# Kernel optimization log

Measured on AMD Instinct MI355X. Metric: run time of the kernel, lower is better.

Reference implementation:

```python
import jax, jax.numpy as jnp
import numpy as np

N, E, F, HID, OUT, B, HEADS = 4096, 131072, 64, 64, 86, 16, 4


def setup_inputs() -> dict:
    key = jax.random.key(0)
    ks = jax.random.split(key, 12)
    s = 0.1
    return {
        "x": jax.random.normal(ks[0], (N, F), dtype=jnp.float32),
        "edge_index": jax.random.randint(ks[1], (2, E), 0, N),
        "edge_attr": jax.random.uniform(ks[2], (E,), dtype=jnp.float32),
        "batch": jnp.sort(jax.random.randint(ks[3], (N,), 0, B)).astype(jnp.int32),
        # GCNConv1: Linear(F -> HID, no bias) + post-aggregation bias
        "W1": jax.random.normal(ks[4], (HID, F), dtype=jnp.float32) * s,
        "b1": jnp.zeros((HID,), jnp.float32),
        # MultiheadAttention(embed_dim=HID, num_heads=4)
        "Win": jax.random.normal(ks[5], (3 * HID, HID), dtype=jnp.float32) * s,
        "b_in": jnp.zeros((3 * HID,), jnp.float32),
        "Wout": jax.random.normal(ks[6], (HID, HID), dtype=jnp.float32) * s,
        "b_out": jnp.zeros((HID,), jnp.float32),
        # GCNConv2: Linear(HID -> OUT)
        "W2": jax.random.normal(ks[7], (OUT, HID), dtype=jnp.float32) * s,
        "b2": jnp.zeros((OUT,), jnp.float32),
    }


def _gcn_layer(h, W, b, src_a, dst_a, norm, n):
    # x' = scatter_add(norm * (x W^T)[src] -> dst) + b   (PyG GCNConv)
    h = h @ W.T
    agg = jax.ops.segment_sum(norm[:, None] * h[src_a], dst_a, num_segments=n)
    return agg + b


def reference(x, edge_index, edge_attr, batch, W1, b1, Win, b_in, Wout, b_out, W2, b2):
    n = x.shape[0]
    # torch.cat([x[:, :-1], x[:, -1:].view(-1,1)], dim=1) == x (identity)
    src, dst = edge_index[0], edge_index[1]
    loop = jnp.arange(n)
    src_a = jnp.concatenate([src, loop])
    dst_a = jnp.concatenate([dst, loop])
    w_a = jnp.concatenate([edge_attr, jnp.ones((n,), x.dtype)])  # self-loops weight 1
    deg = jax.ops.segment_sum(w_a, dst_a, num_segments=n)
    dis = jnp.where(deg > 0, jax.lax.rsqrt(jnp.maximum(deg, 1e-12)), 0.0)
    norm = dis[src_a] * w_a * dis[dst_a]

    h = jax.nn.relu(_gcn_layer(x, W1, b1, src_a, dst_a, norm, n))  # [N, HID]

    # MultiheadAttention over the whole node set as one sequence (batch=1)
    qkv = h @ Win.T + b_in
    q, k, v = jnp.split(qkv, 3, axis=-1)
    dh = HID // HEADS
    to_heads = lambda t: t.reshape(n, HEADS, dh).transpose(1, 0, 2)  # [H, N, dh]
    q, k, v = to_heads(q), to_heads(k), to_heads(v)
    scores = jnp.einsum("hnd,hmd->hnm", q, k) * (1.0 / np.sqrt(dh))
    att = jax.nn.softmax(scores, axis=-1)
    o = jnp.einsum("hnm,hmd->hnd", att, v).transpose(1, 0, 2).reshape(n, HID)
    o = o @ Wout.T + b_out

    h2 = _gcn_layer(o, W2, b2, src_a, dst_a, norm, n)  # [N, OUT]

    # global_mean_pool over graph ids
    sums = jax.ops.segment_sum(h2, batch, num_segments=B)
    cnt = jax.ops.segment_sum(jnp.ones((n,), h2.dtype), batch, num_segments=B)
    return sums / jnp.maximum(cnt, 1.0)[:, None]
```

## Files before the change

### kernel.cpp

```cpp
#include <hip/hip_runtime.h>
#include <hip/hip_bf16.h>

constexpr int N = 4096, E = 131072, OUTF = 86, NB = 16, HEADS = 4, DH = 16;
constexpr int CAP = 128;
constexpr int NSPLIT = 4, KEYS = N / NSPLIT;
constexpr int PCKS = 8;

typedef __attribute__((ext_vector_type(8))) short short8;
typedef __attribute__((ext_vector_type(4))) float f32x4;

constexpr unsigned long long PK_MASK = (1ULL << 40) - 1;
constexpr float PK_SCALE = 1.0f / 16777216.0f;

constexpr size_t OFF_PCK   = 0;
constexpr size_t OFF_INV   = OFF_PCK + 16 * (size_t)N;
constexpr size_t OFF_BUFA  = OFF_INV + 16;
constexpr size_t OFF_QP    = OFF_BUFA + (size_t)N * 64;
constexpr size_t OFF_KP    = OFF_QP + (size_t)N * 32;
constexpr size_t OFF_VP    = OFF_KP + (size_t)N * 32;
constexpr size_t OFF_H2    = OFF_VP + (size_t)N * 32;
constexpr size_t OFF_EPAIR = OFF_H2 + (size_t)N * 86;
constexpr size_t OFF_NORMV = OFF_EPAIR + (size_t)2 * N * CAP;
constexpr size_t OFF_OPART = OFF_NORMV + (size_t)N * CAP;
constexpr size_t OFF_LPART = OFF_OPART + (size_t)HEADS * N * NSPLIT * 16;

__device__ inline unsigned short f2bf(float f) {
    unsigned u = __builtin_bit_cast(unsigned, f);
    u += 0x7FFFu + ((u >> 16) & 1u);
    return (unsigned short)(u >> 16);
}

__device__ inline unsigned pk2bf(float a, float b) {
    __hip_bfloat162 h2 = __float22bfloat162_rn(make_float2(a, b));
    union { __hip_bfloat162 h; unsigned u; } c;
    c.h = h2;
    return c.u;
}

__device__ inline float pk_deg(unsigned long long pk) {
    return (float)(pk & PK_MASK) * PK_SCALE;
}

__global__ __launch_bounds__(256) void d1_kernel(const float* __restrict__ x,
        const float* __restrict__ W1, const int* __restrict__ ei,
        const float* __restrict__ ea, const int* __restrict__ batch,
        const float* __restrict__ b2, float* __restrict__ ws, float* __restrict__ out) {
    __shared__ float4 Ws4[64 * 17];
    __shared__ float4 As4[16 * 17];
    __shared__ int bnd[NB + 1];
    int blk = blockIdx.x, tid = threadIdx.x;
    if (blk < 256) {
        float* bufA = ws + OFF_BUFA;
        for (int idx = tid; idx < 64 * 16; idx += 256)
            Ws4[(idx >> 4) * 17 + (idx & 15)] = ((const float4*)W1)[idx];
        {
            int r = tid >> 4, k4 = tid & 15;
            As4[r * 17 + k4] = ((const float4*)x)[(size_t)(blk * 16 + r) * 16 + k4];
        }
        __syncthreads();
        int r2 = tid & 7, cg = tid >> 3;
        float acc[2][2] = {};
#pragma unroll
        for (int k4 = 0; k4 < 16; ++k4) {
            float4 a0 = As4[r2 * 17 + k4], a1 = As4[(r2 + 8) * 17 + k4];
#pragma unroll
            for (int i = 0; i < 2; ++i) {
                float4 w = Ws4[(cg + 32 * i) * 17 + k4];
                acc[0][i] += a0.x * w.x + a0.y * w.y + a0.z * w.z + a0.w * w.w;
                acc[1][i] += a1.x * w.x + a1.y * w.y + a1.z * w.z + a1.w * w.w;
            }
        }
#pragma unroll
        for (int j = 0; j < 2; ++j)
#pragma unroll
            for (int i = 0; i < 2; ++i)
                bufA[(size_t)(blk * 16 + r2 + 8 * j) * 64 + cg + 32 * i] = acc[j][i];
    } else if (blk < 512) {
        unsigned long long* pck = (unsigned long long*)(ws + OFF_PCK);
        int2* epair = (int2*)(ws + OFF_EPAIR);
        int f = (blk - 256) * 256 + tid;
        int e0 = f, e1 = f + E / 2;
        int s0 = ei[e0], d0 = ei[E + e0];
        int s1 = ei[e1], d1 = ei[E + e1];
        float w0 = ea[e0], w1 = ea[e1];
        unsigned long long a0 = (1ULL << 40) + (unsigned long long)(unsigned)(w0 * 16777216.0f + 0.5f);
        unsigned long long a1 = (1ULL << 40) + (unsigned long long)(unsigned)(w1 * 16777216.0f + 0.5f);
        unsigned long long o0 = atomicAdd(&pck[(size_t)d0 * PCKS], a0);
        unsigned long long o1 = atomicAdd(&pck[(size_t)d1 * PCKS], a1);
        int p0 = (int)(o0 >> 40), p1 = (int)(o1 >> 40);
        if (p0 < CAP) epair[(size_t)d0 * CAP + p0] = make_int2(s0, __float_as_int(w0));
        if (p1 < CAP) epair[(size_t)d1 * CAP + p1] = make_int2(s1, __float_as_int(w1));
    } else {
        float* invcnt = ws + OFF_INV;
        if (tid <= NB) {
            int b = tid, lo = 0, hi = N;
            while (lo < hi) { int m = (lo + hi) >> 1; if (batch[m] < b) lo = m + 1; else hi = m; }
            bnd[tid] = lo;
        }
        __syncthreads();
        if (tid < NB) {
            int cnt = bnd[tid + 1] - bnd[tid];
            invcnt[tid] = cnt > 0 ? 1.0f / (float)cnt : 0.0f;
        }
        for (int idx = tid; idx < NB * OUTF; idx += 256) {
            int b = idx / OUTF;
            int cnt = bnd[b + 1] - bnd[b];
            out[idx] = cnt > 0 ? b2[idx - b * OUTF] : 0.0f;
        }
    }
}

__global__ __launch_bounds__(1024) void d23_kernel(const float* __restrict__ Win,
        const float* __restrict__ b1, const float* __restrict__ b_in,
        float* __restrict__ ws) {
    __shared__ float4 Ws4[16 * 200];
    __shared__ float  Af[16 * 68];

    const unsigned long long* pck = (const unsigned long long*)(ws + OFF_PCK);
    const int2*  epair = (const int2*)(ws + OFF_EPAIR);
    float*       normv = ws + OFF_NORMV;
    const float* bufA  = ws + OFF_BUFA;
    unsigned short* Qp = (unsigned short*)(ws + OFF_QP);
    unsigned short* Kp = (unsigned short*)(ws + OFF_KP);
    unsigned short* Vp = (unsigned short*)(ws + OFF_VP);

    const int tid = threadIdx.x, lane = tid & 63, wv = tid >> 6;
    for (int idx = tid; idx < 192 * 16; idx += 1024) {
        int c = idx >> 4, k4 = idx & 15;
        Ws4[k4 * 200 + c] = ((const float4*)Win)[idx];
    }

    const int node = blockIdx.x * 16 + wv;
    {
        const unsigned long long pkn = pck[(size_t)node * PCKS];
        const float di = rsqrtf(pk_deg(pkn) + 1.0f);
        float acc0 = (di * di) * bufA[(size_t)node * 64 + lane];
        float acc1 = 0.f, acc2 = 0.f, acc3 = 0.f;
        const int cnt = min((int)(pkn >> 40), CAP);
        const int2* pe = epair + (size_t)node * CAP;
        for (int base = 0; base < cnt; base += 64) {
            int rem = cnt - base;
            int   sl = 0;
            float nl = 0.f;
            if (lane < rem) {
                int2 e = pe[base + lane];
                sl = e.x;
                float w = __int_as_float(e.y);
                nl = rsqrtf(pk_deg(pck[(size_t)sl * PCKS]) + 1.0f) * w * di;
                normv[(size_t)node * CAP + base + lane] = nl;
            }
            int m = rem < 64 ? rem : 64;
            int j = 0;
            for (; j + 8 <= m; j += 8) {
                int   s0 = __shfl(sl, j),     s1 = __shfl(sl, j + 1);
                int   s2 = __shfl(sl, j + 2), s3 = __shfl(sl, j + 3);
                int   s4 = __shfl(sl, j + 4), s5 = __shfl(sl, j + 5);
                int   s6 = __shfl(sl, j + 6), s7 = __shfl(sl, j + 7);
                float n0 = __shfl(nl, j),     n1 = __shfl(nl, j + 1);
                float n2 = __shfl(nl, j + 2), n3 = __shfl(nl, j + 3);
                float n4 = __shfl(nl, j + 4), n5 = __shfl(nl, j + 5);
                float n6 = __shfl(nl, j + 6), n7 = __shfl(nl, j + 7);
                float v0 = bufA[(size_t)s0 * 64 + lane], v1 = bufA[(size_t)s1 * 64 + lane];
                float v2 = bufA[(size_t)s2 * 64 + lane], v3 = bufA[(size_t)s3 * 64 + lane];
                float v4 = bufA[(size_t)s4 * 64 + lane], v5 = bufA[(size_t)s5 * 64 + lane];
                float v6 = bufA[(size_t)s6 * 64 + lane], v7 = bufA[(size_t)s7 * 64 + lane];
                acc0 += n0 * v0; acc1 += n1 * v1; acc2 += n2 * v2; acc3 += n3 * v3;
                acc0 += n4 * v4; acc1 += n5 * v5; acc2 += n6 * v6; acc3 += n7 * v7;
            }
            for (; j + 4 <= m; j += 4) {
                int   s0 = __shfl(sl, j),     s1 = __shfl(sl, j + 1);
                int   s2 = __shfl(sl, j + 2), s3 = __shfl(sl, j + 3);
                float n0 = __shfl(nl, j),     n1 = __shfl(nl, j + 1);
                float n2 = __shfl(nl, j + 2), n3 = __shfl(nl, j + 3);
                acc0 += n0 * bufA[(size_t)s0 * 64 + lane];
                acc1 += n1 * bufA[(size_t)s1 * 64 + lane];
                acc2 += n2 * bufA[(size_t)s2 * 64 + lane];
                acc3 += n3 * bufA[(size_t)s3 * 64 + lane];
            }
            for (; j < m; ++j) {
                int   s0 = __shfl(sl, j);
                float n0 = __shfl(nl, j);
                acc0 += n0 * bufA[(size_t)s0 * 64 + lane];
            }
        }
        Af[wv * 68 + lane] = fmaxf((acc0 + acc1) + (acc2 + acc3) + b1[lane], 0.0f);
    }
    __syncthreads();

    {
        const float4* Af4 = (const float4*)Af;
        float acc[3];
#pragma unroll
        for (int i = 0; i < 3; ++i) acc[i] = b_in[lane + 64 * i];
#pragma unroll
        for (int k4 = 0; k4 < 16; ++k4) {
            float4 a = Af4[wv * 17 + k4];
#pragma unroll
            for (int i = 0; i < 3; ++i) {
                float4 w = Ws4[k4 * 200 + lane + 64 * i];
                acc[i] += a.x * w.x + a.y * w.y + a.z * w.z + a.w * w.w;
            }
        }
        const int row = node;
#pragma unroll
        for (int i = 0; i < 3; ++i) {
            int c = lane + 64 * i;
            float v = acc[i];
            if (c < 64) {
                int h = c >> 4, d = c & 15;
                Qp[((size_t)h * N + row) * 16 + d] = f2bf(v * 0.25f);
            } else if (c < 128) {
                int c2 = c - 64, h = c2 >> 4, d = c2 & 15;
                Kp[((size_t)h * N + row) * 16 + d] = f2bf(v);
            } else {
                int c2 = c - 128, h = c2 >> 4, d = c2 & 15;
                Vp[((size_t)h * 16 + d) * N + row] = f2bf(v);
            }
        }
    }
}

__global__ __launch_bounds__(1024) void attn_kernel(const float* __restrict__ ws_c,
        float* __restrict__ ws) {
    __shared__ __align__(16) unsigned short Ksh[64 * 24];
    __shared__ __align__(16) unsigned short Vsh[16 * 80];
    __shared__ __align__(16) unsigned short Plds[16 * 640];

    const unsigned short* Qp = (const unsigned short*)(ws_c + OFF_QP);
    const unsigned short* Kp = (const unsigned short*)(ws_c + OFF_KP);
    const unsigned short* Vp = (const unsigned short*)(ws_c + OFF_VP);
    float* opart = ws + OFF_OPART;
    float* lpart = ws + OFF_LPART;

    const int h  = blockIdx.y;
    const int sp = blockIdx.z;
    const int k0 = sp * KEYS;
    const int tid = threadIdx.x;
    const int lane = tid & 63, wv = tid >> 6;
    const int q15 = lane & 15, quad = lane >> 4;

    const int qbase = blockIdx.x * 256 + wv * 16;
    short8 qf = {};
    if (quad < 2)
        qf = *(const short8*)&Qp[((size_t)h * N + qbase + q15) * 16 + quad * 8];

    f32x4 O = {0.f, 0.f, 0.f, 0.f};
    float l = 0.f;
    unsigned short* Pw = &Plds[wv * 640];
    const unsigned short* Kh = Kp + (size_t)h * N * 16;
    const unsigned short* Vh = Vp + (size_t)h * 16 * N;

    const int krow = tid >> 3, kp = tid & 7;
    const int vd = tid >> 6, vk = tid & 63;

    for (int s = 0; s < KEYS / 64; ++s) {
        __syncthreads();
        if (tid < 512)
            *(short2*)&Ksh[krow * 24 + kp * 2] =
                *(const short2*)&Kh[(size_t)(k0 + s * 64 + krow) * 16 + kp * 2];
        Vsh[vd * 80 + vk] = Vh[(size_t)vd * N + k0 + s * 64 + vk];
        __syncthreads();
#pragma unroll
        for (int t2 = 0; t2 < 2; ++t2) {
#pragma unroll
            for (int t = 0; t < 2; ++t) {
                short8 kf = {};
                if (quad < 2)
                    kf = *(const short8*)&Ksh[(t2 * 32 + t * 16 + q15) * 24 + quad * 8];
                f32x4 zero = {0.f, 0.f, 0.f, 0.f};
                f32x4 sc = __builtin_amdgcn_mfma_f32_16x16x32_bf16(kf, qf, zero, 0, 0, 0);
                float p0 = __expf(sc[0]), p1 = __expf(sc[1]);
                float p2 = __expf(sc[2]), p3 = __expf(sc[3]);
                l += (p0 + p1) + (p2 + p3);
                uint2 pk;
                pk.x = pk2bf(p0, p1);
                pk.y = pk2bf(p2, p3);
                *(uint2*)&Pw[q15 * 40 + t * 16 + quad * 4] = pk;
            }
            asm volatile("s_waitcnt lgkmcnt(0)" ::: "memory");
            short8 pf = *(const short8*)&Pw[q15 * 40 + quad * 8];
            short8 vf = *(const short8*)&Vsh[q15 * 80 + t2 * 32 + quad * 8];
            O = __builtin_amdgcn_mfma_f32_16x16x32_bf16(pf, vf, O, 0, 0, 0);
        }
    }

    l += __shfl_xor(l, 16);
    l += __shfl_xor(l, 32);
    if (lane < 16)
        lpart[((size_t)h * N + qbase + q15) * NSPLIT + sp] = l;
#pragma unroll
    for (int r = 0; r < 4; ++r) {
        int query = qbase + quad * 4 + r;
        opart[(((size_t)h * N + query) * NSPLIT + sp) * 16 + q15] = O[r];
    }
}

__global__ __launch_bounds__(256) void d4b_kernel(const float* __restrict__ Wout,
        const float* __restrict__ b_out, const float* __restrict__ W2,
        float* __restrict__ ws) {
    __shared__ float4 WoS[64 * 17];
    __shared__ float4 W2S[96 * 17];
    __shared__ float  o_sh[16 * 68];
    __shared__ float  Bf[16 * 68];

    const float* opart = ws + OFF_OPART;
    const float* lpart = ws + OFF_LPART;
    float* h2pre = ws + OFF_H2;

    const int tid = threadIdx.x, qbase = blockIdx.x * 16;
    for (int idx = tid; idx < 64 * 16; idx += 256)
        WoS[(idx >> 4) * 17 + (idx & 15)] = ((const float4*)Wout)[idx];
    for (int idx = tid; idx < 86 * 16; idx += 256)
        W2S[(idx >> 4) * 17 + (idx & 15)] = ((const float4*)W2)[idx];

    for (int idx = tid; idx < 16 * 64; idx += 256) {
        int r = idx >> 6, f = idx & 63;
        int h = f >> 4, d = f & 15;
        size_t base = ((size_t)h * N + qbase + r) * NSPLIT;
        float L = 0.f, acc = 0.f;
#pragma unroll
        for (int s = 0; s < NSPLIT; ++s) {
            L += lpart[base + s];
            acc += opart[(base + s) * 16 + d];
        }
        o_sh[r * 68 + f] = acc / L;
    }
    __syncthreads();
    {
        int r = tid & 15, c0 = tid >> 4;
        float4* o4 = (float4*)o_sh;
#pragma unroll
        for (int i = 0; i < 4; ++i) {
            int c = c0 + 16 * i;
            float acc = b_out[c];
#pragma unroll
            for (int k4 = 0; k4 < 16; ++k4) {
                float4 a = o4[r * 17 + k4];
                float4 w = WoS[c * 17 + k4];
                acc += a.x * w.x + a.y * w.y + a.z * w.z + a.w * w.w;
            }
            Bf[r * 68 + c] = acc;
        }
    }
    __syncthreads();
    {
        int r = tid & 15, c0 = tid >> 4;
        float4* B4 = (float4*)Bf;
#pragma unroll
        for (int i = 0; i < 6; ++i) {
            int c = c0 + 16 * i;
            if (c < OUTF) {
                float acc = 0.f;
#pragma unroll
                for (int k4 = 0; k4 < 16; ++k4) {
                    float4 a = B4[r * 17 + k4];
                    float4 w = W2S[c * 17 + k4];
                    acc += a.x * w.x + a.y * w.y + a.z * w.z + a.w * w.w;
                }
                h2pre[(size_t)(qbase + r) * OUTF + c] = acc;
            }
        }
    }
}

__global__ __launch_bounds__(1024) void d5_kernel(const int* __restrict__ batch,
        float* __restrict__ ws, float* __restrict__ out) {
    __shared__ float vec[16][88];
    __shared__ int   bix[16];

    const unsigned long long* pck = (const unsigned long long*)(ws + OFF_PCK);
    const int2*  epair = (const int2*)(ws + OFF_EPAIR);
    const float* normv = ws + OFF_NORMV;
    const float* invcnt= ws + OFF_INV;
    const float* h2pre = ws + OFF_H2;

    const int tid = threadIdx.x;
    const int lane = tid & 63, wv = tid >> 6;
    const int node = blockIdx.x * 16 + wv;
    const bool hi2 = lane < (OUTF - 64);
    const int b = batch[node];
    const float inv = invcnt[b];
    const unsigned long long pkn = pck[(size_t)node * PCKS];
    const float di2 = 1.0f / (pk_deg(pkn) + 1.0f);
    const float* Hn = h2pre + (size_t)node * OUTF;
    float a0 = di2 * Hn[lane],                  a1 = 0.f, a2 = 0.f, a3 = 0.f;
    float c0 = hi2 ? di2 * Hn[64 + lane] : 0.f, c1 = 0.f, c2 = 0.f, c3 = 0.f;
    const int cnt = min((int)(pkn >> 40), CAP);
    const int2* pe = epair + (size_t)node * CAP;

    for (int base = 0; base < cnt; base += 64) {
        int rem = cnt - base;
        int   sl = 0;
        float nl = 0.f;
        if (lane < rem) {
            sl = pe[base + lane].x;
            nl = normv[(size_t)node * CAP + base + lane];
        }
        int m = rem < 64 ? rem : 64;
        int j = 0;
        for (; j + 8 <= m; j += 8) {
            int   s0 = __shfl(sl, j),     s1 = __shfl(sl, j + 1);
            int   s2 = __shfl(sl, j + 2), s3 = __shfl(sl, j + 3);
            int   s4 = __shfl(sl, j + 4), s5 = __shfl(sl, j + 5);
            int   s6 = __shfl(sl, j + 6), s7 = __shfl(sl, j + 7);
            float n0 = __shfl(nl, j),     n1 = __shfl(nl, j + 1);
            float n2 = __shfl(nl, j + 2), n3 = __shfl(nl, j + 3);
            float n4 = __shfl(nl, j + 4), n5 = __shfl(nl, j + 5);
            float n6 = __shfl(nl, j + 6), n7 = __shfl(nl, j + 7);
            const float* H0 = h2pre + (size_t)s0 * OUTF;
            const float* H1 = h2pre + (size_t)s1 * OUTF;
            const float* H2 = h2pre + (size_t)s2 * OUTF;
            const float* H3 = h2pre + (size_t)s3 * OUTF;
            const float* H4 = h2pre + (size_t)s4 * OUTF;
            const float* H5 = h2pre + (size_t)s5 * OUTF;
            const float* H6 = h2pre + (size_t)s6 * OUTF;
            const float* H7 = h2pre + (size_t)s7 * OUTF;
            float v0 = H0[lane], v1 = H1[lane], v2 = H2[lane], v3 = H3[lane];
            float v4 = H4[lane], v5 = H5[lane], v6 = H6[lane], v7 = H7[lane];
            a0 += n0 * v0; a1 += n1 * v1; a2 += n2 * v2; a3 += n3 * v3;
            a0 += n4 * v4; a1 += n5 * v5; a2 += n6 * v6; a3 += n7 * v7;
            if (hi2) {
                float w0 = H0[64 + lane], w1 = H1[64 + lane];
                float w2 = H2[64 + lane], w3 = H3[64 + lane];
                float w4 = H4[64 + lane], w5 = H5[64 + lane];
                float w6 = H6[64 + lane], w7 = H7[64 + lane];
                c0 += n0 * w0; c1 += n1 * w1; c2 += n2 * w2; c3 += n3 * w3;
                c0 += n4 * w4; c1 += n5 * w5; c2 += n6 * w6; c3 += n7 * w7;
            }
        }
        for (; j + 4 <= m; j += 4) {
            int   s0 = __shfl(sl, j),     s1 = __shfl(sl, j + 1);
            int   s2 = __shfl(sl, j + 2), s3 = __shfl(sl, j + 3);
            float n0 = __shfl(nl, j),     n1 = __shfl(nl, j + 1);
            float n2 = __shfl(nl, j + 2), n3 = __shfl(nl, j + 3);
            const float* H0 = h2pre + (size_t)s0 * OUTF;
            const float* H1 = h2pre + (size_t)s1 * OUTF;
            const float* H2 = h2pre + (size_t)s2 * OUTF;
            const float* H3 = h2pre + (size_t)s3 * OUTF;
            a0 += n0 * H0[lane]; if (hi2) c0 += n0 * H0[64 + lane];
            a1 += n1 * H1[lane]; if (hi2) c1 += n1 * H1[64 + lane];
            a2 += n2 * H2[lane]; if (hi2) c2 += n2 * H2[64 + lane];
            a3 += n3 * H3[lane]; if (hi2) c3 += n3 * H3[64 + lane];
        }
        for (; j < m; ++j) {
            int   s0 = __shfl(sl, j);
            float n0 = __shfl(nl, j);
            const float* H0 = h2pre + (size_t)s0 * OUTF;
            a0 += n0 * H0[lane];
            if (hi2) c0 += n0 * H0[64 + lane];
        }
    }
    vec[wv][lane] = ((a0 + a1) + (a2 + a3)) * inv;
    if (hi2) vec[wv][64 + lane] = ((c0 + c1) + (c2 + c3)) * inv;
    if (lane == 0) bix[wv] = b;
    __syncthreads();
    if (tid < OUTF) {
        int curb = bix[0];
        float acc = 0.f;
#pragma unroll
        for (int w = 0; w < 16; ++w) {
            int bw = bix[w];
            if (bw != curb) {
                atomicAdd(&out[curb * OUTF + tid], acc);
                curb = bw; acc = 0.f;
            }
            acc += vec[w][tid];
        }
        atomicAdd(&out[curb * OUTF + tid], acc);
    }
}

extern "C" void kernel_launch(void* const* d_in, const int* in_sizes, int n_in,
                              void* d_out, int out_size, void* d_ws, size_t ws_size,
                              hipStream_t stream) {
    const float* x     = (const float*)d_in[0];
    const int*   ei    = (const int*)  d_in[1];
    const float* ea    = (const float*)d_in[2];
    const int*   batch = (const int*)  d_in[3];
    const float* W1    = (const float*)d_in[4];
    const float* b1    = (const float*)d_in[5];
    const float* Win   = (const float*)d_in[6];
    const float* b_in  = (const float*)d_in[7];
    const float* Wout  = (const float*)d_in[8];
    const float* b_out = (const float*)d_in[9];
    const float* W2    = (const float*)d_in[10];
    const float* b2    = (const float*)d_in[11];
    float* out = (float*)d_out;
    float* ws  = (float*)d_ws;

    hipMemsetAsync(ws + OFF_PCK, 0, (size_t)N * 64, stream);
    d1_kernel<<<513, 256, 0, stream>>>(x, W1, ei, ea, batch, b2, ws, out);
    d23_kernel<<<N / 16, 1024, 0, stream>>>(Win, b1, b_in, ws);
    attn_kernel<<<dim3(N / 256, HEADS, NSPLIT), 1024, 0, stream>>>(ws, ws);
    d4b_kernel<<<N / 16, 256, 0, stream>>>(Wout, b_out, W2, ws);
    d5_kernel<<<N / 16, 1024, 0, stream>>>(batch, ws, out);
}
```

Before: 148.8 us.

## Double-buffer attention K/V tiles, use exp2 softmax, stage edge lists in LDS

The attention kernel now prefetches the next K/V tile into registers while computing on the current one and writes it into a second LDS buffer. This removes one of the two barriers per iteration and overlaps global loads with MFMA work. Q is pre-scaled by log2(e) so the softmax can use the hardware exp2 instruction instead of __expf. In the two GCN aggregation kernels, the per-edge source index and norm are staged in per-wave LDS and read back with broadcast loads instead of many __shfl calls. This adds LDS use and register pressure.

```diff
diff --git a/kernel.cpp b/kernel.cpp
--- a/kernel.cpp
+++ b/kernel.cpp
@@ -11,6 +11,7 @@
 
 constexpr unsigned long long PK_MASK = (1ULL << 40) - 1;
 constexpr float PK_SCALE = 1.0f / 16777216.0f;
+constexpr float QSCALE = 0.25f * 1.44269504088896340736f;
 
 constexpr size_t OFF_PCK   = 0;
 constexpr size_t OFF_INV   = OFF_PCK + 16 * (size_t)N;
@@ -115,6 +116,7 @@
         float* __restrict__ ws) {
     __shared__ float4 Ws4[16 * 200];
     __shared__ float  Af[16 * 68];
+    __shared__ int2   Ed[16][64];
 
     const unsigned long long* pck = (const unsigned long long*)(ws + OFF_PCK);
     const int2*  epair = (const int2*)(ws + OFF_EPAIR);
@@ -149,38 +151,26 @@
                 nl = rsqrtf(pk_deg(pck[(size_t)sl * PCKS]) + 1.0f) * w * di;
                 normv[(size_t)node * CAP + base + lane] = nl;
             }
+            Ed[wv][lane] = make_int2(sl, __float_as_int(nl));
             int m = rem < 64 ? rem : 64;
             int j = 0;
             for (; j + 8 <= m; j += 8) {
-                int   s0 = __shfl(sl, j),     s1 = __shfl(sl, j + 1);
-                int   s2 = __shfl(sl, j + 2), s3 = __shfl(sl, j + 3);
-                int   s4 = __shfl(sl, j + 4), s5 = __shfl(sl, j + 5);
-                int   s6 = __shfl(sl, j + 6), s7 = __shfl(sl, j + 7);
-                float n0 = __shfl(nl, j),     n1 = __shfl(nl, j + 1);
-                float n2 = __shfl(nl, j + 2), n3 = __shfl(nl, j + 3);
-                float n4 = __shfl(nl, j + 4), n5 = __shfl(nl, j + 5);
-                float n6 = __shfl(nl, j + 6), n7 = __shfl(nl, j + 7);
-                float v0 = bufA[(size_t)s0 * 64 + lane], v1 = bufA[(size_t)s1 * 64 + lane];
-                float v2 = bufA[(size_t)s2 * 64 + lane], v3 = bufA[(size_t)s3 * 64 + lane];
-                float v4 = bufA[(size_t)s4 * 64 + lane], v5 = bufA[(size_t)s5 * 64 + lane];
-                float v6 = bufA[(size_t)s6 * 64 + lane], v7 = bufA[(size_t)s7 * 64 + lane];
-                acc0 += n0 * v0; acc1 += n1 * v1; acc2 += n2 * v2; acc3 += n3 * v3;
-                acc0 += n4 * v4; acc1 += n5 * v5; acc2 += n6 * v6; acc3 += n7 * v7;
-            }
-            for (; j + 4 <= m; j += 4) {
-                int   s0 = __shfl(sl, j),     s1 = __shfl(sl, j + 1);
-                int   s2 = __shfl(sl, j + 2), s3 = __shfl(sl, j + 3);
-                float n0 = __shfl(nl, j),     n1 = __shfl(nl, j + 1);
-                float n2 = __shfl(nl, j + 2), n3 = __shfl(nl, j + 3);
-                acc0 += n0 * bufA[(size_t)s0 * 64 + lane];
-                acc1 += n1 * bufA[(size_t)s1 * 64 + lane];
-                acc2 += n2 * bufA[(size_t)s2 * 64 + lane];
-                acc3 += n3 * bufA[(size_t)s3 * 64 + lane];
+                int2 e0 = Ed[wv][j],     e1 = Ed[wv][j + 1];
+                int2 e2 = Ed[wv][j + 2], e3 = Ed[wv][j + 3];
+                int2 e4 = Ed[wv][j + 4], e5 = Ed[wv][j + 5];
+                int2 e6 = Ed[wv][j + 6], e7 = Ed[wv][j + 7];
+                float v0 = bufA[(size_t)e0.x * 64 + lane], v1 = bufA[(size_t)e1.x * 64 + lane];
+                float v2 = bufA[(size_t)e2.x * 64 + lane], v3 = bufA[(size_t)e3.x * 64 + lane];
+                float v4 = bufA[(size_t)e4.x * 64 + lane], v5 = bufA[(size_t)e5.x * 64 + lane];
+                float v6 = bufA[(size_t)e6.x * 64 + lane], v7 = bufA[(size_t)e7.x * 64 + lane];
+                acc0 += __int_as_float(e0.y) * v0; acc1 += __int_as_float(e1.y) * v1;
+                acc2 += __int_as_float(e2.y) * v2; acc3 += __int_as_float(e3.y) * v3;
+                acc0 += __int_as_float(e4.y) * v4; acc1 += __int_as_float(e5.y) * v5;
+                acc2 += __int_as_float(e6.y) * v6; acc3 += __int_as_float(e7.y) * v7;
             }
             for (; j < m; ++j) {
-                int   s0 = __shfl(sl, j);
-                float n0 = __shfl(nl, j);
-                acc0 += n0 * bufA[(size_t)s0 * 64 + lane];
+                int2 e0 = Ed[wv][j];
+                acc0 += __int_as_float(e0.y) * bufA[(size_t)e0.x * 64 + lane];
             }
         }
         Af[wv * 68 + lane] = fmaxf((acc0 + acc1) + (acc2 + acc3) + b1[lane], 0.0f);
@@ -208,7 +198,7 @@
             float v = acc[i];
             if (c < 64) {
                 int h = c >> 4, d = c & 15;
-                Qp[((size_t)h * N + row) * 16 + d] = f2bf(v * 0.25f);
+                Qp[((size_t)h * N + row) * 16 + d] = f2bf(v * QSCALE);
             } else if (c < 128) {
                 int c2 = c - 64, h = c2 >> 4, d = c2 & 15;
                 Kp[((size_t)h * N + row) * 16 + d] = f2bf(v);
@@ -222,8 +212,8 @@
 
 __global__ __launch_bounds__(1024) void attn_kernel(const float* __restrict__ ws_c,
         float* __restrict__ ws) {
-    __shared__ __align__(16) unsigned short Ksh[64 * 24];
-    __shared__ __align__(16) unsigned short Vsh[16 * 80];
+    __shared__ __align__(16) unsigned short Ksh[2][64 * 24];
+    __shared__ __align__(16) unsigned short Vsh[2][16 * 80];
     __shared__ __align__(16) unsigned short Plds[16 * 640];
 
     const unsigned short* Qp = (const unsigned short*)(ws_c + OFF_QP);
@@ -253,24 +243,37 @@
     const int krow = tid >> 3, kp = tid & 7;
     const int vd = tid >> 6, vk = tid & 63;
 
+    short2 kr = {};
+    unsigned short vr;
+    if (tid < 512)
+        kr = *(const short2*)&Kh[(size_t)(k0 + krow) * 16 + kp * 2];
+    vr = Vh[(size_t)vd * N + k0 + vk];
+    if (tid < 512)
+        *(short2*)&Ksh[0][krow * 24 + kp * 2] = kr;
+    Vsh[0][vd * 80 + vk] = vr;
+    __syncthreads();
+
+    int cur = 0;
     for (int s = 0; s < KEYS / 64; ++s) {
-        __syncthreads();
-        if (tid < 512)
-            *(short2*)&Ksh[krow * 24 + kp * 2] =
-                *(const short2*)&Kh[(size_t)(k0 + s * 64 + krow) * 16 + kp * 2];
-        Vsh[vd * 80 + vk] = Vh[(size_t)vd * N + k0 + s * 64 + vk];
-        __syncthreads();
+        const bool hasnext = (s + 1 < KEYS / 64);
+        if (hasnext) {
+            if (tid < 512)
+                kr = *(const short2*)&Kh[(size_t)(k0 + (s + 1) * 64 + krow) * 16 + kp * 2];
+            vr = Vh[(size_t)vd * N + k0 + (s + 1) * 64 + vk];
+        }
+        const unsigned short* Kc = Ksh[cur];
+        const unsigned short* Vc = Vsh[cur];
 #pragma unroll
         for (int t2 = 0; t2 < 2; ++t2) {
 #pragma unroll
             for (int t = 0; t < 2; ++t) {
                 short8 kf = {};
                 if (quad < 2)
-                    kf = *(const short8*)&Ksh[(t2 * 32 + t * 16 + q15) * 24 + quad * 8];
+                    kf = *(const short8*)&Kc[(t2 * 32 + t * 16 + q15) * 24 + quad * 8];
                 f32x4 zero = {0.f, 0.f, 0.f, 0.f};
                 f32x4 sc = __builtin_amdgcn_mfma_f32_16x16x32_bf16(kf, qf, zero, 0, 0, 0);
-                float p0 = __expf(sc[0]), p1 = __expf(sc[1]);
-                float p2 = __expf(sc[2]), p3 = __expf(sc[3]);
+                float p0 = __builtin_amdgcn_exp2f(sc[0]), p1 = __builtin_amdgcn_exp2f(sc[1]);
+                float p2 = __builtin_amdgcn_exp2f(sc[2]), p3 = __builtin_amdgcn_exp2f(sc[3]);
                 l += (p0 + p1) + (p2 + p3);
                 uint2 pk;
                 pk.x = pk2bf(p0, p1);
@@ -279,9 +282,16 @@
             }
             asm volatile("s_waitcnt lgkmcnt(0)" ::: "memory");
             short8 pf = *(const short8*)&Pw[q15 * 40 + quad * 8];
-            short8 vf = *(const short8*)&Vsh[q15 * 80 + t2 * 32 + quad * 8];
+            short8 vf = *(const short8*)&Vc[q15 * 80 + t2 * 32 + quad * 8];
             O = __builtin_amdgcn_mfma_f32_16x16x32_bf16(pf, vf, O, 0, 0, 0);
         }
+        if (hasnext) {
+            if (tid < 512)
+                *(short2*)&Ksh[cur ^ 1][krow * 24 + kp * 2] = kr;
+            Vsh[cur ^ 1][vd * 80 + vk] = vr;
+        }
+        __syncthreads();
+        cur ^= 1;
     }
 
     l += __shfl_xor(l, 16);
@@ -367,6 +377,7 @@
         float* __restrict__ ws, float* __restrict__ out) {
     __shared__ float vec[16][88];
     __shared__ int   bix[16];
+    __shared__ int2  Ed[16][64];
 
     const unsigned long long* pck = (const unsigned long long*)(ws + OFF_PCK);
     const int2*  epair = (const int2*)(ws + OFF_EPAIR);
@@ -396,25 +407,26 @@
             sl = pe[base + lane].x;
             nl = normv[(size_t)node * CAP + base + lane];
         }
+        Ed[wv][lane] = make_int2(sl, __float_as_int(nl));
         int m = rem < 64 ? rem : 64;
         int j = 0;
         for (; j + 8 <= m; j += 8) {
-            int   s0 = __shfl(sl, j),     s1 = __shfl(sl, j + 1);
-            int   s2 = __shfl(sl, j + 2), s3 = __shfl(sl, j + 3);
-            int   s4 = __shfl(sl, j + 4), s5 = __shfl(sl, j + 5);
-            int   s6 = __shfl(sl, j + 6), s7 = __shfl(sl, j + 7);
-            float n0 = __shfl(nl, j),     n1 = __shfl(nl, j + 1);
-            float n2 = __shfl(nl, j + 2), n3 = __shfl(nl, j + 3);
-            float n4 = __shfl(nl, j + 4), n5 = __shfl(nl, j + 5);
-            float n6 = __shfl(nl, j + 6), n7 = __shfl(nl, j + 7);
-            const float* H0 = h2pre + (size_t)s0 * OUTF;
-            const float* H1 = h2pre + (size_t)s1 * OUTF;
-            const float* H2 = h2pre + (size_t)s2 * OUTF;
-            const float* H3 = h2pre + (size_t)s3 * OUTF;
-            const float* H4 = h2pre + (size_t)s4 * OUTF;
-            const float* H5 = h2pre + (size_t)s5 * OUTF;
-            const float* H6 = h2pre + (size_t)s6 * OUTF;
-            const float* H7 = h2pre + (size_t)s7 * OUTF;
+            int2 e0 = Ed[wv][j],     e1 = Ed[wv][j + 1];
+            int2 e2 = Ed[wv][j + 2], e3 = Ed[wv][j + 3];
+            int2 e4 = Ed[wv][j + 4], e5 = Ed[wv][j + 5];
+            int2 e6 = Ed[wv][j + 6], e7 = Ed[wv][j + 7];
+            const float* H0 = h2pre + (size_t)e0.x * OUTF;
+            const float* H1 = h2pre + (size_t)e1.x * OUTF;
+            const float* H2 = h2pre + (size_t)e2.x * OUTF;
+            const float* H3 = h2pre + (size_t)e3.x * OUTF;
+            const float* H4 = h2pre + (size_t)e4.x * OUTF;
+            const float* H5 = h2pre + (size_t)e5.x * OUTF;
+            const float* H6 = h2pre + (size_t)e6.x * OUTF;
+            const float* H7 = h2pre + (size_t)e7.x * OUTF;
+            float n0 = __int_as_float(e0.y), n1 = __int_as_float(e1.y);
+            float n2 = __int_as_float(e2.y), n3 = __int_as_float(e3.y);
+            float n4 = __int_as_float(e4.y), n5 = __int_as_float(e5.y);
+            float n6 = __int_as_float(e6.y), n7 = __int_as_float(e7.y);
             float v0 = H0[lane], v1 = H1[lane], v2 = H2[lane], v3 = H3[lane];
             float v4 = H4[lane], v5 = H5[lane], v6 = H6[lane], v7 = H7[lane];
             a0 += n0 * v0; a1 += n1 * v1; a2 += n2 * v2; a3 += n3 * v3;
@@ -428,24 +440,10 @@
                 c0 += n4 * w4; c1 += n5 * w5; c2 += n6 * w6; c3 += n7 * w7;
             }
         }
-        for (; j + 4 <= m; j += 4) {
-            int   s0 = __shfl(sl, j),     s1 = __shfl(sl, j + 1);
-            int   s2 = __shfl(sl, j + 2), s3 = __shfl(sl, j + 3);
-            float n0 = __shfl(nl, j),     n1 = __shfl(nl, j + 1);
-            float n2 = __shfl(nl, j + 2), n3 = __shfl(nl, j + 3);
-            const float* H0 = h2pre + (size_t)s0 * OUTF;
-            const float* H1 = h2pre + (size_t)s1 * OUTF;
-            const float* H2 = h2pre + (size_t)s2 * OUTF;
-            const float* H3 = h2pre + (size_t)s3 * OUTF;
-            a0 += n0 * H0[lane]; if (hi2) c0 += n0 * H0[64 + lane];
-            a1 += n1 * H1[lane]; if (hi2) c1 += n1 * H1[64 + lane];
-            a2 += n2 * H2[lane]; if (hi2) c2 += n2 * H2[64 + lane];
-            a3 += n3 * H3[lane]; if (hi2) c3 += n3 * H3[64 + lane];
-        }
         for (; j < m; ++j) {
-            int   s0 = __shfl(sl, j);
-            float n0 = __shfl(nl, j);
-            const float* H0 = h2pre + (size_t)s0 * OUTF;
+            int2 e0 = Ed[wv][j];
+            const float* H0 = h2pre + (size_t)e0.x * OUTF;
+            float n0 = __int_as_float(e0.y);
             a0 += n0 * H0[lane];
             if (hi2) c0 += n0 * H0[64 + lane];
         }
@@ -488,7 +486,7 @@
     float* out = (float*)d_out;
     float* ws  = (float*)d_ws;
 
-    hipMemsetAsync(ws + OFF_PCK, 0, (size_t)N * 64, stream);
+    (void)hipMemsetAsync(ws + OFF_PCK, 0, (size_t)N * 64, stream);
     d1_kernel<<<513, 256, 0, stream>>>(x, W1, ei, ea, batch, b2, ws, out);
     d23_kernel<<<N / 16, 1024, 0, stream>>>(Win, b1, b_in, ws);
     attn_kernel<<<dim3(N / 256, HEADS, NSPLIT), 1024, 0, stream>>>(ws, ws);
```

New measurement: 139.0 us. 1.07x faster.
